# Kernel optimization log

Hardware: AMD Instinct MI355X
Metric: run time of the kernel (lower is better)

## Reference

```python
import jax, jax.numpy as jnp
import numpy as np

H = 16            # num heads (sharded)
NOPE = 128        # qk_nope_head_dim
ROPE = 64         # qk_rope_head_dim
VD = 128          # v_head_dim
KV_RANK = 512
HEAD = NOPE + ROPE  # 192
SCALE = HEAD ** (-0.5)  # mscale == 1 (no yarn scaling)
EPS = 1e-6


def rmsnorm(x, w):
    var = jnp.mean(x * x, axis=-1, keepdims=True)
    return x * jax.lax.rsqrt(var + EPS) * w


def apply_rope(pe, cos, sin):
    # pe: [T, h, ROPE]; torch code de-interleaves pairs then applies
    # non-interleaved (rotate-half) rope: out = [e*cos - o*sin, o*cos + e*sin]
    e = pe[..., 0::2]
    o = pe[..., 1::2]
    c = cos[:, None, :]
    s = sin[:, None, :]
    return jnp.concatenate([e * c - o * s, o * c + e * s], axis=-1)


def setup_inputs() -> dict:
    key = jax.random.key(0)
    ks = jax.random.split(key, 10)
    T, D = 4096, 2048
    w = 0.02
    return {
        "hidden_states": jax.random.normal(ks[0], (T, D), jnp.float32),
        "cos": jax.random.uniform(ks[1], (T, ROPE // 2), jnp.float32),
        "sin": jax.random.uniform(ks[2], (T, ROPE // 2), jnp.float32),
        "w_q_a": jax.random.normal(ks[3], (D, 1536), jnp.float32) * w,
        "q_a_ln_w": jnp.ones((1536,), jnp.float32),
        "w_q_b": jax.random.normal(ks[4], (1536, H * HEAD), jnp.float32) * w,
        "w_kv_a": jax.random.normal(ks[5], (D, KV_RANK + ROPE), jnp.float32) * w,
        "kv_a_ln_w": jnp.ones((KV_RANK,), jnp.float32),
        "w_kv_b": jax.random.normal(ks[6], (KV_RANK, H * (NOPE + VD)), jnp.float32) * w,
        "w_o": jax.random.normal(ks[7], (H * VD, D), jnp.float32) * w,
        "batch_size": 2,
    }


def reference(hidden_states, cos, sin, w_q_a, q_a_ln_w, w_q_b, w_kv_a,
              kv_a_ln_w, w_kv_b, w_o, batch_size):
    T, D = hidden_states.shape
    B = int(batch_size)
    S = T // B

    # Q: low-rank down proj -> RMSNorm -> up proj
    q = rmsnorm(hidden_states @ w_q_a, q_a_ln_w) @ w_q_b
    q = q.reshape(T, H, HEAD)
    q_nope = q[..., :NOPE]
    q_pe = apply_rope(q[..., NOPE:], cos, sin)

    # KV: joint down proj with shared rope part (MQA-style)
    ckv = hidden_states @ w_kv_a                        # [T, 512+64]
    compressed_kv = ckv[:, :KV_RANK]
    k_pe = apply_rope(ckv[:, KV_RANK:][:, None, :], cos, sin)  # [T, 1, 64]
    kv = (rmsnorm(compressed_kv, kv_a_ln_w) @ w_kv_b).reshape(T, H, NOPE + VD)
    k_nope = kv[..., :NOPE]
    v = kv[..., NOPE:]                                   # [T, H, 128]

    # Assemble full query/key heads (value pad to 192 + final slice is a no-op
    # mathematically since padded dims are zero; we keep value dim = 128).
    query = jnp.concatenate([q_nope, q_pe], axis=-1)     # [T, H, 192]
    key = jnp.concatenate([k_nope, jnp.broadcast_to(k_pe, (T, H, ROPE))], axis=-1)

    # Causal (prefill) attention per sequence
    qb = query.reshape(B, S, H, HEAD)
    kb = key.reshape(B, S, H, HEAD)
    vb = v.reshape(B, S, H, VD)
    scores = jnp.einsum("bqhd,bkhd->bhqk", qb, kb) * SCALE
    causal = jnp.tril(jnp.ones((S, S), bool))
    scores = jnp.where(causal, scores, jnp.finfo(scores.dtype).min)
    probs = jax.nn.softmax(scores, axis=-1)
    attn = jnp.einsum("bhqk,bkhd->bqhd", probs, vb)      # [B, S, H, 128]

    return attn.reshape(T, H * VD) @ w_o
```

## Files before the change

### kernel.cpp

```cpp
#include <hip/hip_runtime.h>
#include <cstdint>
#include <cstddef>

#define TT 4096
#define DD 2048
#define NH 16
#define HEADD 192
#define NOPE 128
#define VDIM 128
#define SEQ 2048

typedef __bf16 bf16x8 __attribute__((ext_vector_type(8)));
typedef float f32x4 __attribute__((ext_vector_type(4)));
typedef unsigned int u32;

__device__ __forceinline__ float bf2f(unsigned short u) {
    union { unsigned int i; float f; } v; v.i = ((unsigned int)u) << 16; return v.f;
}
__device__ __forceinline__ unsigned short f2bf(float f) {
    union { float f; unsigned int i; } v; v.f = f;
    unsigned int r = v.i + 0x7FFFu + ((v.i >> 16) & 1u);
    return (unsigned short)(r >> 16);
}
__device__ __forceinline__ void gload16(const unsigned short* g, unsigned short* l) {
    __builtin_amdgcn_global_load_lds((const __attribute__((address_space(1))) u32*)g,
                                     (__attribute__((address_space(3))) u32*)l, 16, 0, 0);
}

__global__ __launch_bounds__(256) void cvt_bf16_k(const float* __restrict__ x,
                                                  unsigned short* __restrict__ y, int n) {
    int i = (blockIdx.x * 256 + threadIdx.x) * 4;
    if (i < n) {
        float4 v = *(const float4*)(x + i);
        uint2 o;
        o.x = (unsigned int)f2bf(v.x) | ((unsigned int)f2bf(v.y) << 16);
        o.y = (unsigned int)f2bf(v.z) | ((unsigned int)f2bf(v.w) << 16);
        *(uint2*)(y + i) = o;
    }
}

__global__ __launch_bounds__(256) void transpose_cvt_k(const float* __restrict__ W,
                                                       unsigned short* __restrict__ Wt,
                                                       int K, int N) {
    __shared__ float tile[32][33];
    int n0 = blockIdx.x * 32, k0 = blockIdx.y * 32;
    int t = threadIdx.x, lr = t >> 5, lc = t & 31;
#pragma unroll
    for (int p = 0; p < 4; p++) {
        int k = k0 + lr + p * 8, n = n0 + lc;
        tile[lr + p * 8][lc] = (k < K && n < N) ? W[(size_t)k * N + n] : 0.f;
    }
    __syncthreads();
#pragma unroll
    for (int p = 0; p < 4; p++) {
        int n = n0 + lr + p * 8, k = k0 + lc;
        if (n < N && k < K) Wt[(size_t)n * K + k] = f2bf(tile[lc][lr + p * 8]);
    }
}

__global__ __launch_bounds__(256) void gemm_bf16_k(const unsigned short* __restrict__ A,
                                                   const unsigned short* __restrict__ Bt,
                                                   float* __restrict__ C,
                                                   int M, int N, int K) {
    __shared__ __align__(16) unsigned short As[128 * 32];
    __shared__ __align__(16) unsigned short Bs[128 * 32];
    int bm = blockIdx.y * 128, bn = blockIdx.x * 128;
    int t = threadIdx.x;
    int wave = t >> 6, lane = t & 63;
    int wr = (wave >> 1) * 64, wc = (wave & 1) * 64;
    int l15 = lane & 15, quad = lane >> 4;
    f32x4 acc[4][4];
    f32x4 zero = {0.f, 0.f, 0.f, 0.f};
#pragma unroll
    for (int i = 0; i < 4; i++)
#pragma unroll
        for (int j = 0; j < 4; j++) acc[i][j] = zero;
    int r0 = 16 * (2 * wave) + (lane >> 2);
    int cOff = (lane & 3) * 8;
    const unsigned short* gA0 = A + (size_t)(bm + r0) * K + cOff;
    const unsigned short* gA1 = A + (size_t)(bm + r0 + 16) * K + cOff;
    const unsigned short* gB0 = Bt + (size_t)(bn + r0) * K + cOff;
    const unsigned short* gB1 = Bt + (size_t)(bn + r0 + 16) * K + cOff;
    unsigned short* lA0 = &As[(2 * wave) * 512];
    unsigned short* lA1 = &As[(2 * wave + 1) * 512];
    unsigned short* lB0 = &Bs[(2 * wave) * 512];
    unsigned short* lB1 = &Bs[(2 * wave + 1) * 512];
    for (int k0 = 0; k0 < K; k0 += 32) {
        gload16(gA0 + k0, lA0);
        gload16(gA1 + k0, lA1);
        gload16(gB0 + k0, lB0);
        gload16(gB1 + k0, lB1);
        __syncthreads();
        bf16x8 af[4], bfr[4];
#pragma unroll
        for (int i = 0; i < 4; i++)
            af[i] = *(const bf16x8*)&As[(wr + i * 16 + l15) * 32 + quad * 8];
#pragma unroll
        for (int j = 0; j < 4; j++)
            bfr[j] = *(const bf16x8*)&Bs[(wc + j * 16 + l15) * 32 + quad * 8];
#pragma unroll
        for (int i = 0; i < 4; i++)
#pragma unroll
            for (int j = 0; j < 4; j++)
                acc[i][j] = __builtin_amdgcn_mfma_f32_16x16x32_bf16(af[i], bfr[j], acc[i][j], 0, 0, 0);
        __syncthreads();
    }
#pragma unroll
    for (int i = 0; i < 4; i++) {
        int row = bm + wr + i * 16 + quad * 4;
#pragma unroll
        for (int j = 0; j < 4; j++) {
            int col = bn + wc + j * 16 + l15;
            if (col < N) {
                float* cp = C + (size_t)row * N + col;
#pragma unroll
                for (int r = 0; r < 4; r++) cp[(size_t)r * N] = acc[i][j][r];
            }
        }
    }
}

__global__ __launch_bounds__(256) void rmsnorm_k(const float* __restrict__ x,
                                                 const float* __restrict__ w,
                                                 unsigned short* __restrict__ y, int cols) {
    int row = blockIdx.x, t = threadIdx.x;
    const float* xr = x + (size_t)row * cols;
    float s = 0.f;
    for (int i = t; i < cols; i += 256) { float v = xr[i]; s += v * v; }
    __shared__ float red[256];
    red[t] = s; __syncthreads();
    for (int o = 128; o > 0; o >>= 1) { if (t < o) red[t] += red[t + o]; __syncthreads(); }
    float scale = rsqrtf(red[0] / (float)cols + 1e-6f);
    unsigned short* yr = y + (size_t)row * cols;
    for (int i = t; i < cols; i += 256) yr[i] = f2bf(xr[i] * scale * w[i]);
}

__global__ __launch_bounds__(256) void kvprep_k(const float* __restrict__ ckv,
                                                const float* __restrict__ w,
                                                const float* __restrict__ cosb,
                                                const float* __restrict__ sinb,
                                                unsigned short* __restrict__ ckvn,
                                                unsigned short* __restrict__ kpe) {
    int row = blockIdx.x, t = threadIdx.x;
    const float* xr = ckv + (size_t)row * 576;
    float s = 0.f;
#pragma unroll
    for (int i = t; i < 512; i += 256) { float v = xr[i]; s += v * v; }
    __shared__ float red[256];
    red[t] = s; __syncthreads();
    for (int o = 128; o > 0; o >>= 1) { if (t < o) red[t] += red[t + o]; __syncthreads(); }
    float scale = rsqrtf(red[0] / 512.f + 1e-6f);
    unsigned short* yr = ckvn + (size_t)row * 512;
#pragma unroll
    for (int i = t; i < 512; i += 256) yr[i] = f2bf(xr[i] * scale * w[i]);
    if (t < 32) {
        float e = xr[512 + 2 * t], o = xr[512 + 2 * t + 1];
        float c = cosb[row * 32 + t], sn = sinb[row * 32 + t];
        kpe[row * 64 + t]      = f2bf(e * c - o * sn);
        kpe[row * 64 + 32 + t] = f2bf(o * c + e * sn);
    }
}

__global__ __launch_bounds__(256) void qprep_k(const float* __restrict__ q,
                                               const float* __restrict__ cosb,
                                               const float* __restrict__ sinb,
                                               unsigned short* __restrict__ Qb) {
    const float SCALE = 0.07216878364870323f;
    int trow = blockIdx.x, t = threadIdx.x;
    const float* qr = q + (size_t)trow * (NH * HEADD);
    unsigned short* yr = Qb + (size_t)trow * (NH * HEADD);
    for (int i = t; i < NH * HEADD; i += 256) {
        int h = i / HEADD, d = i - h * HEADD;
        float val;
        if (d < NOPE) val = qr[i];
        else {
            int j = d - NOPE;
            int jj = j & 31;
            const float* pe = qr + h * HEADD + NOPE;
            float e = pe[2 * jj], o = pe[2 * jj + 1];
            float c = cosb[trow * 32 + jj], sn = sinb[trow * 32 + jj];
            val = (j < 32) ? (e * c - o * sn) : (o * c + e * sn);
        }
        yr[i] = f2bf(val * SCALE);
    }
}

#define KS_STRIDE 200
#define VT_STRIDE 72
#define P_STRIDE  72

__global__ __launch_bounds__(256) void kprep_k(const float* __restrict__ kvb,
                                               const unsigned short* __restrict__ kpe,
                                               unsigned short* __restrict__ Kb2) {
    int trow = blockIdx.x, t = threadIdx.x;
    int b = trow >> 11, s = trow & 2047;
    int ktile = s >> 6, srow = s & 63;
    const float* kr = kvb + (size_t)trow * 4096;
    for (int i = t; i < NH * HEADD; i += 256) {
        int h = i / HEADD, d = i - h * HEADD;
        unsigned short v = (d < NOPE) ? f2bf(kr[h * 256 + d]) : kpe[trow * 64 + (d - NOPE)];
        Kb2[(((size_t)(b * NH + h) * 32 + ktile) * 64 + srow) * KS_STRIDE + d] = v;
    }
}

__global__ __launch_bounds__(256) void vtrans_k(const float* __restrict__ kvb,
                                                unsigned short* __restrict__ Vt2) {
    __shared__ unsigned short tile[64][132];
    int st = blockIdx.x, h = blockIdx.y, b = blockIdx.z;
    int t = threadIdx.x;
    int s0 = b * SEQ + st * 64;
    for (int c = t; c < 64 * 32; c += 256) {
        int r = c >> 5, d4 = (c & 31) * 4;
        float4 v = *(const float4*)(kvb + (size_t)(s0 + r) * 4096 + h * 256 + NOPE + d4);
        tile[r][d4]     = f2bf(v.x);
        tile[r][d4 + 1] = f2bf(v.y);
        tile[r][d4 + 2] = f2bf(v.z);
        tile[r][d4 + 3] = f2bf(v.w);
    }
    __syncthreads();
    int bh = b * NH + h;
    for (int c = t; c < 128 * 16; c += 256) {
        int d = c >> 4, s4 = (c & 15) * 4;
        unsigned short p0 = tile[s4][d], p1 = tile[s4 + 1][d];
        unsigned short p2 = tile[s4 + 2][d], p3 = tile[s4 + 3][d];
        uint2 o;
        o.x = (unsigned int)p0 | ((unsigned int)p1 << 16);
        o.y = (unsigned int)p2 | ((unsigned int)p3 << 16);
        *(uint2*)(Vt2 + (((size_t)bh * 32 + st) * 128 + d) * VT_STRIDE + s4) = o;
    }
}

__global__ __launch_bounds__(512) void attn_mfma_k(const unsigned short* __restrict__ Qb,
                                                   const unsigned short* __restrict__ Kb2,
                                                   const unsigned short* __restrict__ Vt2,
                                                   unsigned short* __restrict__ Opart,
                                                   float* __restrict__ Mbuf,
                                                   float* __restrict__ Lbuf) {
    __shared__ __align__(16) unsigned short Ks[64 * KS_STRIDE];
    __shared__ __align__(16) unsigned short Vts[128 * VT_STRIDE];
    __shared__ __align__(16) unsigned short Pw[8 * 16 * P_STRIDE];
    int xe = 39 - blockIdx.x;
    int h  = blockIdx.y;
    int b  = blockIdx.z;
    int qt = 0, accn = 0;
    while (true) { int c = (qt >> 2) + 1; if (xe < accn + c) break; accn += c; qt++; }
    int chunk = xe - accn;
    int t = threadIdx.x;
    int w = t >> 6, lane = t & 63;
    int l15 = lane & 15, quad = lane >> 4;
    int bh = b * NH + h;
    int q0 = b * SEQ + qt * 128;
    int qloc = qt * 128 + w * 16 + quad * 4;
    int flat = bh * 40 + xe;

    bf16x8 qf[6];
    {
        const unsigned short* qbase = Qb + ((size_t)(q0 + w * 16 + l15) * NH + h) * HEADD + quad * 8;
#pragma unroll
        for (int c = 0; c < 6; c++)
            qf[c] = *(const bf16x8*)(qbase + c * 32);
    }
    f32x4 acc_o[8];
    f32x4 zero = {0.f, 0.f, 0.f, 0.f};
#pragma unroll
    for (int j = 0; j < 8; j++) acc_o[j] = zero;
    float mrun[4], lrun[4];
#pragma unroll
    for (int r = 0; r < 4; r++) { mrun[r] = -1e30f; lrun[r] = 0.f; }

    unsigned short* Pme = Pw + w * 16 * P_STRIDE;
    int kt0 = chunk * 8, kt1 = min(kt0 + 7, 2 * qt + 1);
    int cbeg = w * 5 + min(w, 3), cnt = (w < 3) ? 6 : 5;
    for (int kt = kt0; kt <= kt1; kt++) {
        __syncthreads();
        {
            const unsigned short* kg = Kb2 + ((size_t)bh * 32 + kt) * (64 * KS_STRIDE) + lane * 8;
            const unsigned short* vg = Vt2 + ((size_t)bh * 32 + kt) * (128 * VT_STRIDE) + lane * 8;
            for (int c = cbeg; c < cbeg + cnt; c++) {
                if (c < 25) gload16(kg + c * 512, &Ks[c * 512]);
                else        gload16(vg + (c - 25) * 512, &Vts[(c - 25) * 512]);
            }
        }
        __syncthreads();
        f32x4 acc_s[4];
#pragma unroll
        for (int j = 0; j < 4; j++) acc_s[j] = zero;
#pragma unroll
        for (int c = 0; c < 6; c++) {
#pragma unroll
            for (int j = 0; j < 4; j++) {
                bf16x8 kf = *(const bf16x8*)&Ks[(j * 16 + l15) * KS_STRIDE + c * 32 + quad * 8];
                acc_s[j] = __builtin_amdgcn_mfma_f32_16x16x32_bf16(qf[c], kf, acc_s[j], 0, 0, 0);
            }
        }
        float sv[4][4];
#pragma unroll
        for (int j = 0; j < 4; j++) {
            int kcol = kt * 64 + j * 16 + l15;
#pragma unroll
            for (int r = 0; r < 4; r++)
                sv[j][r] = (kcol > qloc + r) ? -1e30f : acc_s[j][r];
        }
        float alpha[4];
#pragma unroll
        for (int r = 0; r < 4; r++) {
            float v = fmaxf(fmaxf(sv[0][r], sv[1][r]), fmaxf(sv[2][r], sv[3][r]));
            v = fmaxf(v, __shfl_xor(v, 1));
            v = fmaxf(v, __shfl_xor(v, 2));
            v = fmaxf(v, __shfl_xor(v, 4));
            v = fmaxf(v, __shfl_xor(v, 8));
            float mnew = fmaxf(mrun[r], v);
            alpha[r] = __expf(mrun[r] - mnew);
            mrun[r] = mnew;
            float rs = 0.f;
#pragma unroll
            for (int j = 0; j < 4; j++) { float p = __expf(sv[j][r] - mnew); sv[j][r] = p; rs += p; }
            rs += __shfl_xor(rs, 1);
            rs += __shfl_xor(rs, 2);
            rs += __shfl_xor(rs, 4);
            rs += __shfl_xor(rs, 8);
            lrun[r] = lrun[r] * alpha[r] + rs;
        }
#pragma unroll
        for (int j = 0; j < 4; j++)
#pragma unroll
            for (int r = 0; r < 4; r++)
                Pme[(quad * 4 + r) * P_STRIDE + j * 16 + l15] = f2bf(sv[j][r]);
#pragma unroll
        for (int jt = 0; jt < 8; jt++)
#pragma unroll
            for (int r = 0; r < 4; r++) acc_o[jt][r] *= alpha[r];
#pragma unroll
        for (int c2 = 0; c2 < 2; c2++) {
            bf16x8 pf = *(const bf16x8*)&Pme[l15 * P_STRIDE + c2 * 32 + quad * 8];
#pragma unroll
            for (int jt = 0; jt < 8; jt++) {
                bf16x8 vf = *(const bf16x8*)&Vts[(jt * 16 + l15) * VT_STRIDE + c2 * 32 + quad * 8];
                acc_o[jt] = __builtin_amdgcn_mfma_f32_16x16x32_bf16(pf, vf, acc_o[jt], 0, 0, 0);
            }
        }
    }
#pragma unroll
    for (int r = 0; r < 4; r++) {
        int row = w * 16 + quad * 4 + r;
        unsigned short* op = Opart + (size_t)flat * 16384 + row * 128 + l15;
#pragma unroll
        for (int jt = 0; jt < 8; jt++)
            op[jt * 16] = f2bf(acc_o[jt][r]);
        if (l15 == 0) {
            Mbuf[(size_t)flat * 128 + row] = mrun[r];
            Lbuf[(size_t)flat * 128 + row] = lrun[r];
        }
    }
}

__global__ __launch_bounds__(256) void attn_combine_k(const unsigned short* __restrict__ Opart,
                                                      const float* __restrict__ Mbuf,
                                                      const float* __restrict__ Lbuf,
                                                      unsigned short* __restrict__ attnb) {
    int q64 = blockIdx.x, h = blockIdx.y, b = blockIdx.z;
    int qt = q64 >> 1, half = q64 & 1;
    int nch = (qt >> 2) + 1;
    int F = 0;
    for (int q = 0; q < qt; q++) F += (q >> 2) + 1;
    int flat0 = (b * NH + h) * 40 + F;
    int t = threadIdx.x;
    int row = t >> 2, d0 = (t & 3) * 32;
    int row128 = half * 64 + row;
    float mc[4], lc[4], wgt[4];
    float mstar = -1e30f;
#pragma unroll
    for (int c = 0; c < 4; c++) {
        if (c < nch) {
            mc[c] = Mbuf[(size_t)(flat0 + c) * 128 + row128];
            lc[c] = Lbuf[(size_t)(flat0 + c) * 128 + row128];
        } else { mc[c] = -1e30f; lc[c] = 0.f; }
        mstar = fmaxf(mstar, mc[c]);
    }
    float L = 0.f;
#pragma unroll
    for (int c = 0; c < 4; c++) { wgt[c] = __expf(mc[c] - mstar); L += wgt[c] * lc[c]; }
    float invL = 1.f / L;
    float acc[32];
#pragma unroll
    for (int j = 0; j < 32; j++) acc[j] = 0.f;
#pragma unroll
    for (int c = 0; c < 4; c++) {
        if (c < nch) {
            const unsigned short* src = Opart + (size_t)(flat0 + c) * 16384 + row128 * 128 + d0;
            float wc = wgt[c];
#pragma unroll
            for (int g = 0; g < 4; g++) {
                uint4 u = *(const uint4*)(src + g * 8);
                const unsigned short* sp = (const unsigned short*)&u;
#pragma unroll
                for (int j = 0; j < 8; j++) acc[g * 8 + j] += wc * bf2f(sp[j]);
            }
        }
    }
    unsigned short* dst = attnb + (size_t)(b * SEQ + q64 * 64 + row) * 2048 + h * 128 + d0;
#pragma unroll
    for (int g = 0; g < 4; g++) {
        uint4 o;
        unsigned short* sp = (unsigned short*)&o;
#pragma unroll
        for (int j = 0; j < 8; j++) sp[j] = f2bf(acc[g * 8 + j] * invL);
        *(uint4*)(dst + g * 8) = o;
    }
}

extern "C" void kernel_launch(void* const* d_in, const int* in_sizes, int n_in,
                              void* d_out, int out_size, void* d_ws, size_t ws_size,
                              hipStream_t stream) {
    const float* hs     = (const float*)d_in[0];
    const float* cosb   = (const float*)d_in[1];
    const float* sinb   = (const float*)d_in[2];
    const float* w_q_a  = (const float*)d_in[3];
    const float* q_ln   = (const float*)d_in[4];
    const float* w_q_b  = (const float*)d_in[5];
    const float* w_kv_a = (const float*)d_in[6];
    const float* kv_ln  = (const float*)d_in[7];
    const float* w_kv_b = (const float*)d_in[8];
    const float* w_o    = (const float*)d_in[9];
    float* out = (float*)d_out;

    char* base = (char*)d_ws;
    size_t off = 0;
    auto take = [&](size_t bytes) { void* p = base + off; off += (bytes + 255) & ~(size_t)255; return p; };
    unsigned short* wqaT  = (unsigned short*)take((size_t)1536 * 2048 * 2);
    unsigned short* wqbT  = (unsigned short*)take((size_t)3072 * 1536 * 2);
    unsigned short* wkvaT = (unsigned short*)take((size_t)576 * 2048 * 2);
    unsigned short* wkvbT = (unsigned short*)take((size_t)4096 * 512 * 2);
    unsigned short* woT   = (unsigned short*)take((size_t)2048 * 2048 * 2);
    unsigned short* hsb   = (unsigned short*)take((size_t)TT * DD * 2);
    unsigned short* qan   = (unsigned short*)take((size_t)TT * 1536 * 2);
    unsigned short* ckvn  = (unsigned short*)take((size_t)TT * 512 * 2);
    unsigned short* kpe   = (unsigned short*)take((size_t)TT * 64 * 2);
    unsigned short* Qbuf  = (unsigned short*)take((size_t)TT * NH * HEADD * 2);
    unsigned short* Kb2   = (unsigned short*)take((size_t)32 * 32 * 64 * KS_STRIDE * 2);
    unsigned short* Vt2   = (unsigned short*)take((size_t)32 * 32 * 128 * VT_STRIDE * 2);
    unsigned short* attnb = (unsigned short*)take((size_t)TT * 2048 * 2);
    char* Sreg = (char*)take((size_t)TT * 4096 * 4);
    float* S = (float*)Sreg;
    unsigned short* Opart = (unsigned short*)Sreg;
    float* Mbuf = (float*)(Sreg + (size_t)1280 * 16384 * 2);
    float* Lbuf = Mbuf + (size_t)1280 * 128;

    cvt_bf16_k<<<(TT * DD) / 1024, 256, 0, stream>>>(hs, hsb, TT * DD);
    transpose_cvt_k<<<dim3(1536 / 32, 2048 / 32), 256, 0, stream>>>(w_q_a, wqaT, 2048, 1536);
    transpose_cvt_k<<<dim3(3072 / 32, 1536 / 32), 256, 0, stream>>>(w_q_b, wqbT, 1536, 3072);
    transpose_cvt_k<<<dim3(18, 2048 / 32), 256, 0, stream>>>(w_kv_a, wkvaT, 2048, 576);
    transpose_cvt_k<<<dim3(4096 / 32, 512 / 32), 256, 0, stream>>>(w_kv_b, wkvbT, 512, 4096);
    transpose_cvt_k<<<dim3(2048 / 32, 2048 / 32), 256, 0, stream>>>(w_o, woT, 2048, 2048);

    gemm_bf16_k<<<dim3(12, 32), 256, 0, stream>>>(hsb, wqaT, S, 4096, 1536, 2048);
    rmsnorm_k<<<4096, 256, 0, stream>>>(S, q_ln, qan, 1536);
    gemm_bf16_k<<<dim3(5, 32), 256, 0, stream>>>(hsb, wkvaT, S, 4096, 576, 2048);
    kvprep_k<<<4096, 256, 0, stream>>>(S, kv_ln, cosb, sinb, ckvn, kpe);
    gemm_bf16_k<<<dim3(24, 32), 256, 0, stream>>>(qan, wqbT, S, 4096, 3072, 1536);
    qprep_k<<<4096, 256, 0, stream>>>(S, cosb, sinb, Qbuf);
    gemm_bf16_k<<<dim3(32, 32), 256, 0, stream>>>(ckvn, wkvbT, S, 4096, 4096, 512);
    kprep_k<<<4096, 256, 0, stream>>>(S, kpe, Kb2);
    vtrans_k<<<dim3(32, 16, 2), 256, 0, stream>>>(S, Vt2);
    attn_mfma_k<<<dim3(40, 16, 2), 512, 0, stream>>>(Qbuf, Kb2, Vt2, Opart, Mbuf, Lbuf);
    attn_combine_k<<<dim3(32, 16, 2), 256, 0, stream>>>(Opart, Mbuf, Lbuf, attnb);
    gemm_bf16_k<<<dim3(16, 32), 256, 0, stream>>>(attnb, woT, out, 4096, 2048, 2048);
}
```

Measured before the change: 595.2 us.

## Fuse q_a/kv_a projections, emit bf16 GEMM outputs, write K/V layouts from GEMM epilogue

Concatenates w_q_a and w_kv_a into one 2112-column weight, so the hidden states feed a single GEMM instead of two. Intermediate GEMMs now write bf16 instead of fp32, which halves intermediate traffic. The kv_b GEMM epilogue scatters results straight into the attention-ready K tile and transposed V tile layouts, replacing the separate kprep and vtrans kernels. The costs are scattered 2-byte stores in the epilogue, an extra bf16 rounding before RMSNorm and RoPE, and 17 column tiles where the last one is mostly padding.

New measurement: 554.4 us. 6.9% less time.

```diff
diff --git a/kernel.cpp b/kernel.cpp
--- a/kernel.cpp
+++ b/kernel.cpp
@@ -120,113 +120,218 @@
     }
 }
 
-__global__ __launch_bounds__(256) void rmsnorm_k(const float* __restrict__ x,
-                                                 const float* __restrict__ w,
-                                                 unsigned short* __restrict__ y, int cols) {
+__global__ __launch_bounds__(256) void gemm_bf16o_k(const unsigned short* __restrict__ A,
+                                                    const unsigned short* __restrict__ Bt,
+                                                    unsigned short* __restrict__ C,
+                                                    int M, int N, int K) {
+    __shared__ __align__(16) unsigned short As[128 * 32];
+    __shared__ __align__(16) unsigned short Bs[128 * 32];
+    int bm = blockIdx.y * 128, bn = blockIdx.x * 128;
+    int t = threadIdx.x;
+    int wave = t >> 6, lane = t & 63;
+    int wr = (wave >> 1) * 64, wc = (wave & 1) * 64;
+    int l15 = lane & 15, quad = lane >> 4;
+    f32x4 acc[4][4];
+    f32x4 zero = {0.f, 0.f, 0.f, 0.f};
+#pragma unroll
+    for (int i = 0; i < 4; i++)
+#pragma unroll
+        for (int j = 0; j < 4; j++) acc[i][j] = zero;
+    int r0 = 16 * (2 * wave) + (lane >> 2);
+    int cOff = (lane & 3) * 8;
+    const unsigned short* gA0 = A + (size_t)(bm + r0) * K + cOff;
+    const unsigned short* gA1 = A + (size_t)(bm + r0 + 16) * K + cOff;
+    const unsigned short* gB0 = Bt + (size_t)(bn + r0) * K + cOff;
+    const unsigned short* gB1 = Bt + (size_t)(bn + r0 + 16) * K + cOff;
+    unsigned short* lA0 = &As[(2 * wave) * 512];
+    unsigned short* lA1 = &As[(2 * wave + 1) * 512];
+    unsigned short* lB0 = &Bs[(2 * wave) * 512];
+    unsigned short* lB1 = &Bs[(2 * wave + 1) * 512];
+    for (int k0 = 0; k0 < K; k0 += 32) {
+        gload16(gA0 + k0, lA0);
+        gload16(gA1 + k0, lA1);
+        gload16(gB0 + k0, lB0);
+        gload16(gB1 + k0, lB1);
+        __syncthreads();
+        bf16x8 af[4], bfr[4];
+#pragma unroll
+        for (int i = 0; i < 4; i++)
+            af[i] = *(const bf16x8*)&As[(wr + i * 16 + l15) * 32 + quad * 8];
+#pragma unroll
+        for (int j = 0; j < 4; j++)
+            bfr[j] = *(const bf16x8*)&Bs[(wc + j * 16 + l15) * 32 + quad * 8];
+#pragma unroll
+        for (int i = 0; i < 4; i++)
+#pragma unroll
+            for (int j = 0; j < 4; j++)
+                acc[i][j] = __builtin_amdgcn_mfma_f32_16x16x32_bf16(af[i], bfr[j], acc[i][j], 0, 0, 0);
+        __syncthreads();
+    }
+#pragma unroll
+    for (int i = 0; i < 4; i++) {
+        int row = bm + wr + i * 16 + quad * 4;
+#pragma unroll
+        for (int j = 0; j < 4; j++) {
+            int col = bn + wc + j * 16 + l15;
+            if (col < N) {
+                unsigned short* cp = C + (size_t)row * N + col;
+#pragma unroll
+                for (int r = 0; r < 4; r++) cp[(size_t)r * N] = f2bf(acc[i][j][r]);
+            }
+        }
+    }
+}
+
+#define KS_STRIDE 200
+#define VT_STRIDE 72
+#define P_STRIDE  72
+
+__global__ __launch_bounds__(256) void gemm_kv_k(const unsigned short* __restrict__ A,
+                                                 const unsigned short* __restrict__ Bt,
+                                                 unsigned short* __restrict__ Kb2,
+                                                 unsigned short* __restrict__ Vt2) {
+    const int K = 512;
+    __shared__ __align__(16) unsigned short As[128 * 32];
+    __shared__ __align__(16) unsigned short Bs[128 * 32];
+    int bm = blockIdx.y * 128, bn = blockIdx.x * 128;
+    int t = threadIdx.x;
+    int wave = t >> 6, lane = t & 63;
+    int wr = (wave >> 1) * 64, wc = (wave & 1) * 64;
+    int l15 = lane & 15, quad = lane >> 4;
+    f32x4 acc[4][4];
+    f32x4 zero = {0.f, 0.f, 0.f, 0.f};
+#pragma unroll
+    for (int i = 0; i < 4; i++)
+#pragma unroll
+        for (int j = 0; j < 4; j++) acc[i][j] = zero;
+    int r0 = 16 * (2 * wave) + (lane >> 2);
+    int cOff = (lane & 3) * 8;
+    const unsigned short* gA0 = A + (size_t)(bm + r0) * K + cOff;
+    const unsigned short* gA1 = A + (size_t)(bm + r0 + 16) * K + cOff;
+    const unsigned short* gB0 = Bt + (size_t)(bn + r0) * K + cOff;
+    const unsigned short* gB1 = Bt + (size_t)(bn + r0 + 16) * K + cOff;
+    unsigned short* lA0 = &As[(2 * wave) * 512];
+    unsigned short* lA1 = &As[(2 * wave + 1) * 512];
+    unsigned short* lB0 = &Bs[(2 * wave) * 512];
+    unsigned short* lB1 = &Bs[(2 * wave + 1) * 512];
+    for (int k0 = 0; k0 < K; k0 += 32) {
+        gload16(gA0 + k0, lA0);
+        gload16(gA1 + k0, lA1);
+        gload16(gB0 + k0, lB0);
+        gload16(gB1 + k0, lB1);
+        __syncthreads();
+        bf16x8 af[4], bfr[4];
+#pragma unroll
+        for (int i = 0; i < 4; i++)
+            af[i] = *(const bf16x8*)&As[(wr + i * 16 + l15) * 32 + quad * 8];
+#pragma unroll
+        for (int j = 0; j < 4; j++)
+            bfr[j] = *(const bf16x8*)&Bs[(wc + j * 16 + l15) * 32 + quad * 8];
+#pragma unroll
+        for (int i = 0; i < 4; i++)
+#pragma unroll
+            for (int j = 0; j < 4; j++)
+                acc[i][j] = __builtin_amdgcn_mfma_f32_16x16x32_bf16(af[i], bfr[j], acc[i][j], 0, 0, 0);
+        __syncthreads();
+    }
+#pragma unroll
+    for (int j = 0; j < 4; j++) {
+        int col = bn + wc + j * 16 + l15;
+        int h = col >> 8, dd = col & 255;
+#pragma unroll
+        for (int i = 0; i < 4; i++) {
+            int row0 = bm + wr + i * 16 + quad * 4;
+#pragma unroll
+            for (int r = 0; r < 4; r++) {
+                int row = row0 + r;
+                int b = row >> 11, s = row & 2047;
+                int kt = s >> 6, sr = s & 63;
+                size_t bh = (size_t)(b * NH + h);
+                unsigned short v = f2bf(acc[i][j][r]);
+                if (dd < 128)
+                    Kb2[((bh * 32 + kt) * 64 + sr) * KS_STRIDE + dd] = v;
+                else
+                    Vt2[((bh * 32 + kt) * 128 + (dd - 128)) * VT_STRIDE + sr] = v;
+            }
+        }
+    }
+}
+
+__global__ __launch_bounds__(256) void kpe_fill_k(const unsigned short* __restrict__ kpe,
+                                                  unsigned short* __restrict__ Kb2) {
+    int trow = blockIdx.x, t = threadIdx.x;
+    int b = trow >> 11, s = trow & 2047;
+    int kt = s >> 6, sr = s & 63;
+    const unsigned short* src = kpe + trow * 64;
+#pragma unroll
+    for (int i = t; i < NH * 64; i += 256) {
+        int h = i >> 6, d = i & 63;
+        Kb2[(((size_t)(b * NH + h) * 32 + kt) * 64 + sr) * KS_STRIDE + 128 + d] = src[d];
+    }
+}
+
+__global__ __launch_bounds__(256) void rmsnorm_bf_k(const unsigned short* __restrict__ x,
+                                                    const float* __restrict__ w,
+                                                    unsigned short* __restrict__ y) {
     int row = blockIdx.x, t = threadIdx.x;
-    const float* xr = x + (size_t)row * cols;
+    const unsigned short* xr = x + (size_t)row * 2112;
     float s = 0.f;
-    for (int i = t; i < cols; i += 256) { float v = xr[i]; s += v * v; }
+    for (int i = t; i < 1536; i += 256) { float v = bf2f(xr[i]); s += v * v; }
     __shared__ float red[256];
     red[t] = s; __syncthreads();
     for (int o = 128; o > 0; o >>= 1) { if (t < o) red[t] += red[t + o]; __syncthreads(); }
-    float scale = rsqrtf(red[0] / (float)cols + 1e-6f);
-    unsigned short* yr = y + (size_t)row * cols;
-    for (int i = t; i < cols; i += 256) yr[i] = f2bf(xr[i] * scale * w[i]);
-}
-
-__global__ __launch_bounds__(256) void kvprep_k(const float* __restrict__ ckv,
-                                                const float* __restrict__ w,
-                                                const float* __restrict__ cosb,
-                                                const float* __restrict__ sinb,
-                                                unsigned short* __restrict__ ckvn,
-                                                unsigned short* __restrict__ kpe) {
+    float scale = rsqrtf(red[0] / 1536.f + 1e-6f);
+    unsigned short* yr = y + (size_t)row * 1536;
+    for (int i = t; i < 1536; i += 256) yr[i] = f2bf(bf2f(xr[i]) * scale * w[i]);
+}
+
+__global__ __launch_bounds__(256) void kvprep_bf_k(const unsigned short* __restrict__ qab,
+                                                   const float* __restrict__ w,
+                                                   const float* __restrict__ cosb,
+                                                   const float* __restrict__ sinb,
+                                                   unsigned short* __restrict__ ckvn,
+                                                   unsigned short* __restrict__ kpe) {
     int row = blockIdx.x, t = threadIdx.x;
-    const float* xr = ckv + (size_t)row * 576;
+    const unsigned short* xr = qab + (size_t)row * 2112 + 1536;
     float s = 0.f;
 #pragma unroll
-    for (int i = t; i < 512; i += 256) { float v = xr[i]; s += v * v; }
+    for (int i = t; i < 512; i += 256) { float v = bf2f(xr[i]); s += v * v; }
     __shared__ float red[256];
     red[t] = s; __syncthreads();
     for (int o = 128; o > 0; o >>= 1) { if (t < o) red[t] += red[t + o]; __syncthreads(); }
     float scale = rsqrtf(red[0] / 512.f + 1e-6f);
     unsigned short* yr = ckvn + (size_t)row * 512;
 #pragma unroll
-    for (int i = t; i < 512; i += 256) yr[i] = f2bf(xr[i] * scale * w[i]);
+    for (int i = t; i < 512; i += 256) yr[i] = f2bf(bf2f(xr[i]) * scale * w[i]);
     if (t < 32) {
-        float e = xr[512 + 2 * t], o = xr[512 + 2 * t + 1];
+        float e = bf2f(xr[512 + 2 * t]), o = bf2f(xr[512 + 2 * t + 1]);
         float c = cosb[row * 32 + t], sn = sinb[row * 32 + t];
         kpe[row * 64 + t]      = f2bf(e * c - o * sn);
         kpe[row * 64 + 32 + t] = f2bf(o * c + e * sn);
     }
 }
 
-__global__ __launch_bounds__(256) void qprep_k(const float* __restrict__ q,
-                                               const float* __restrict__ cosb,
-                                               const float* __restrict__ sinb,
-                                               unsigned short* __restrict__ Qb) {
+__global__ __launch_bounds__(256) void qprep_bf_k(const unsigned short* __restrict__ q,
+                                                  const float* __restrict__ cosb,
+                                                  const float* __restrict__ sinb,
+                                                  unsigned short* __restrict__ Qb) {
     const float SCALE = 0.07216878364870323f;
     int trow = blockIdx.x, t = threadIdx.x;
-    const float* qr = q + (size_t)trow * (NH * HEADD);
+    const unsigned short* qr = q + (size_t)trow * (NH * HEADD);
     unsigned short* yr = Qb + (size_t)trow * (NH * HEADD);
     for (int i = t; i < NH * HEADD; i += 256) {
         int h = i / HEADD, d = i - h * HEADD;
         float val;
-        if (d < NOPE) val = qr[i];
+        if (d < NOPE) val = bf2f(qr[i]);
         else {
             int j = d - NOPE;
             int jj = j & 31;
-            const float* pe = qr + h * HEADD + NOPE;
-            float e = pe[2 * jj], o = pe[2 * jj + 1];
+            const unsigned short* pe = qr + h * HEADD + NOPE;
+            float e = bf2f(pe[2 * jj]), o = bf2f(pe[2 * jj + 1]);
             float c = cosb[trow * 32 + jj], sn = sinb[trow * 32 + jj];
             val = (j < 32) ? (e * c - o * sn) : (o * c + e * sn);
         }
         yr[i] = f2bf(val * SCALE);
-    }
-}
-
-#define KS_STRIDE 200
-#define VT_STRIDE 72
-#define P_STRIDE  72
-
-__global__ __launch_bounds__(256) void kprep_k(const float* __restrict__ kvb,
-                                               const unsigned short* __restrict__ kpe,
-                                               unsigned short* __restrict__ Kb2) {
-    int trow = blockIdx.x, t = threadIdx.x;
-    int b = trow >> 11, s = trow & 2047;
-    int ktile = s >> 6, srow = s & 63;
-    const float* kr = kvb + (size_t)trow * 4096;
-    for (int i = t; i < NH * HEADD; i += 256) {
-        int h = i / HEADD, d = i - h * HEADD;
-        unsigned short v = (d < NOPE) ? f2bf(kr[h * 256 + d]) : kpe[trow * 64 + (d - NOPE)];
-        Kb2[(((size_t)(b * NH + h) * 32 + ktile) * 64 + srow) * KS_STRIDE + d] = v;
-    }
-}
-
-__global__ __launch_bounds__(256) void vtrans_k(const float* __restrict__ kvb,
-                                                unsigned short* __restrict__ Vt2) {
-    __shared__ unsigned short tile[64][132];
-    int st = blockIdx.x, h = blockIdx.y, b = blockIdx.z;
-    int t = threadIdx.x;
-    int s0 = b * SEQ + st * 64;
-    for (int c = t; c < 64 * 32; c += 256) {
-        int r = c >> 5, d4 = (c & 31) * 4;
-        float4 v = *(const float4*)(kvb + (size_t)(s0 + r) * 4096 + h * 256 + NOPE + d4);
-        tile[r][d4]     = f2bf(v.x);
-        tile[r][d4 + 1] = f2bf(v.y);
-        tile[r][d4 + 2] = f2bf(v.z);
-        tile[r][d4 + 3] = f2bf(v.w);
-    }
-    __syncthreads();
-    int bh = b * NH + h;
-    for (int c = t; c < 128 * 16; c += 256) {
-        int d = c >> 4, s4 = (c & 15) * 4;
-        unsigned short p0 = tile[s4][d], p1 = tile[s4 + 1][d];
-        unsigned short p2 = tile[s4 + 2][d], p3 = tile[s4 + 3][d];
-        uint2 o;
-        o.x = (unsigned int)p0 | ((unsigned int)p1 << 16);
-        o.y = (unsigned int)p2 | ((unsigned int)p3 << 16);
-        *(uint2*)(Vt2 + (((size_t)bh * 32 + st) * 128 + d) * VT_STRIDE + s4) = o;
     }
 }
 
@@ -427,41 +532,38 @@
     char* base = (char*)d_ws;
     size_t off = 0;
     auto take = [&](size_t bytes) { void* p = base + off; off += (bytes + 255) & ~(size_t)255; return p; };
-    unsigned short* wqaT  = (unsigned short*)take((size_t)1536 * 2048 * 2);
+    unsigned short* wqabT = (unsigned short*)take((size_t)2112 * 2048 * 2);
     unsigned short* wqbT  = (unsigned short*)take((size_t)3072 * 1536 * 2);
-    unsigned short* wkvaT = (unsigned short*)take((size_t)576 * 2048 * 2);
     unsigned short* wkvbT = (unsigned short*)take((size_t)4096 * 512 * 2);
     unsigned short* woT   = (unsigned short*)take((size_t)2048 * 2048 * 2);
     unsigned short* hsb   = (unsigned short*)take((size_t)TT * DD * 2);
+    unsigned short* qab   = (unsigned short*)take((size_t)TT * 2112 * 2);
     unsigned short* qan   = (unsigned short*)take((size_t)TT * 1536 * 2);
     unsigned short* ckvn  = (unsigned short*)take((size_t)TT * 512 * 2);
     unsigned short* kpe   = (unsigned short*)take((size_t)TT * 64 * 2);
+    unsigned short* qb3   = (unsigned short*)take((size_t)TT * 3072 * 2);
     unsigned short* Qbuf  = (unsigned short*)take((size_t)TT * NH * HEADD * 2);
     unsigned short* Kb2   = (unsigned short*)take((size_t)32 * 32 * 64 * KS_STRIDE * 2);
     unsigned short* Vt2   = (unsigned short*)take((size_t)32 * 32 * 128 * VT_STRIDE * 2);
     unsigned short* attnb = (unsigned short*)take((size_t)TT * 2048 * 2);
-    char* Sreg = (char*)take((size_t)TT * 4096 * 4);
-    float* S = (float*)Sreg;
-    unsigned short* Opart = (unsigned short*)Sreg;
-    float* Mbuf = (float*)(Sreg + (size_t)1280 * 16384 * 2);
-    float* Lbuf = Mbuf + (size_t)1280 * 128;
+    unsigned short* Opart = (unsigned short*)take((size_t)1280 * 16384 * 2);
+    float* Mbuf = (float*)take((size_t)1280 * 128 * 4);
+    float* Lbuf = (float*)take((size_t)1280 * 128 * 4);
 
     cvt_bf16_k<<<(TT * DD) / 1024, 256, 0, stream>>>(hs, hsb, TT * DD);
-    transpose_cvt_k<<<dim3(1536 / 32, 2048 / 32), 256, 0, stream>>>(w_q_a, wqaT, 2048, 1536);
+    transpose_cvt_k<<<dim3(1536 / 32, 2048 / 32), 256, 0, stream>>>(w_q_a, wqabT, 2048, 1536);
+    transpose_cvt_k<<<dim3(18, 2048 / 32), 256, 0, stream>>>(w_kv_a, wqabT + (size_t)1536 * 2048, 2048, 576);
     transpose_cvt_k<<<dim3(3072 / 32, 1536 / 32), 256, 0, stream>>>(w_q_b, wqbT, 1536, 3072);
-    transpose_cvt_k<<<dim3(18, 2048 / 32), 256, 0, stream>>>(w_kv_a, wkvaT, 2048, 576);
     transpose_cvt_k<<<dim3(4096 / 32, 512 / 32), 256, 0, stream>>>(w_kv_b, wkvbT, 512, 4096);
     transpose_cvt_k<<<dim3(2048 / 32, 2048 / 32), 256, 0, stream>>>(w_o, woT, 2048, 2048);
 
-    gemm_bf16_k<<<dim3(12, 32), 256, 0, stream>>>(hsb, wqaT, S, 4096, 1536, 2048);
-    rmsnorm_k<<<4096, 256, 0, stream>>>(S, q_ln, qan, 1536);
-    gemm_bf16_k<<<dim3(5, 32), 256, 0, stream>>>(hsb, wkvaT, S, 4096, 576, 2048);
-    kvprep_k<<<4096, 256, 0, stream>>>(S, kv_ln, cosb, sinb, ckvn, kpe);
-    gemm_bf16_k<<<dim3(24, 32), 256, 0, stream>>>(qan, wqbT, S, 4096, 3072, 1536);
-    qprep_k<<<4096, 256, 0, stream>>>(S, cosb, sinb, Qbuf);
-    gemm_bf16_k<<<dim3(32, 32), 256, 0, stream>>>(ckvn, wkvbT, S, 4096, 4096, 512);
-    kprep_k<<<4096, 256, 0, stream>>>(S, kpe, Kb2);
-    vtrans_k<<<dim3(32, 16, 2), 256, 0, stream>>>(S, Vt2);
+    gemm_bf16o_k<<<dim3(17, 32), 256, 0, stream>>>(hsb, wqabT, qab, 4096, 2112, 2048);
+    rmsnorm_bf_k<<<4096, 256, 0, stream>>>(qab, q_ln, qan);
+    kvprep_bf_k<<<4096, 256, 0, stream>>>(qab, kv_ln, cosb, sinb, ckvn, kpe);
+    gemm_bf16o_k<<<dim3(24, 32), 256, 0, stream>>>(qan, wqbT, qb3, 4096, 3072, 1536);
+    qprep_bf_k<<<4096, 256, 0, stream>>>(qb3, cosb, sinb, Qbuf);
+    gemm_kv_k<<<dim3(32, 32), 256, 0, stream>>>(ckvn, wkvbT, Kb2, Vt2);
+    kpe_fill_k<<<4096, 256, 0, stream>>>(kpe, Kb2);
     attn_mfma_k<<<dim3(40, 16, 2), 512, 0, stream>>>(Qbuf, Kb2, Vt2, Opart, Mbuf, Lbuf);
     attn_combine_k<<<dim3(32, 16, 2), 256, 0, stream>>>(Opart, Mbuf, Lbuf, attnb);
     gemm_bf16_k<<<dim3(16, 32), 256, 0, stream>>>(attnb, woT, out, 4096, 2048, 2048);
```
